# Performance work log

Hardware: AMD Instinct MI355X
Metric: run time of the kernel (lower is better)

The kernel has to match this reference:

```python
import jax, jax.numpy as jnp
import numpy as np

N, K, D = 32768, 8192, 256


def setup_inputs() -> dict:
    key = jax.random.key(0)
    k1, k2 = jax.random.split(key)
    x = jax.random.normal(k1, (N, D), dtype=jnp.float32)
    vectors = jax.random.normal(k2, (K, D), dtype=jnp.float32)  # codebook
    return {"x": x, "vectors": vectors}


def reference(x, vectors):
    # torch.cdist(x[:,None,:], vectors[None]) followed by argmin over K.
    # Euclidean distance is monotone in squared distance, so argmin over the
    # without a sqrt, matching the original math exactly for the returned ids.
    x2 = jnp.sum(x * x, axis=-1, keepdims=True)          # [N, 1]
    c2 = jnp.sum(vectors * vectors, axis=-1)             # [K]
    d2 = x2 + c2 - 2.0 * jnp.matmul(x, vectors.T)        # [N, K]
    indices = jnp.argmin(d2, axis=-1)                    # [N]
    return indices.astype(jnp.int32)
```

## Files before the change

kernel.cpp:

```cpp
#include <hip/hip_runtime.h>
#include <stdint.h>
#include <stddef.h>


#define N_PTS 32768
#define K_CB  8192
#define D_DIM 256
#define TM 128
#define TN 128
#define SPLITK 4
#define KCHUNK (K_CB / SPLITK)
#define NTILES (KCHUNK / TN)
#define NCHUNKS (NTILES * 8)

#define WS_XH   0
#define WS_XL   (WS_XH + N_PTS * D_DIM * 2)
#define WS_CH   (WS_XL + N_PTS * D_DIM * 2)
#define WS_CL   (WS_CH + K_CB * D_DIM * 2)
#define WS_C2   (WS_CL + K_CB * D_DIM * 2)
#define WS_PD   (WS_C2 + K_CB * 4)
#define WS_PI   (WS_PD + SPLITK * N_PTS * 4)
#define WS_END  (WS_PI + SPLITK * N_PTS * 4)

typedef _Float16 half4v __attribute__((ext_vector_type(4)));
typedef _Float16 half8v __attribute__((ext_vector_type(8)));
typedef float    f32x4  __attribute__((ext_vector_type(4)));

__device__ __forceinline__ void gld16(const void* g, void* l) {
    __builtin_amdgcn_global_load_lds(
        (const __attribute__((address_space(1))) void*)g,
        (__attribute__((address_space(3))) void*)l, 16, 0, 0);
}


#define XBLOCKS (N_PTS * D_DIM / 4 / 256)
#define CBLOCKS (K_CB * D_DIM / 4 / 256)

__global__ void __launch_bounds__(256)
prep_kernel(const float* __restrict__ x, const float* __restrict__ vecs,
            _Float16* __restrict__ xh, _Float16* __restrict__ xl,
            _Float16* __restrict__ ch, _Float16* __restrict__ cl,
            float* __restrict__ c2) {
    const int b = blockIdx.x;
    if (b < XBLOCKS) {
        const int i = b * 256 + threadIdx.x;
        const float4 v = ((const float4*)x)[i];
        half4v h = {(_Float16)v.x, (_Float16)v.y, (_Float16)v.z, (_Float16)v.w};
        half4v l = {(_Float16)((v.x - (float)h[0]) * 2048.0f),
                    (_Float16)((v.y - (float)h[1]) * 2048.0f),
                    (_Float16)((v.z - (float)h[2]) * 2048.0f),
                    (_Float16)((v.w - (float)h[3]) * 2048.0f)};
        *(half4v*)(xh + (size_t)i * 4) = h;
        *(half4v*)(xl + (size_t)i * 4) = l;
    } else {
        const int i = (b - XBLOCKS) * 256 + threadIdx.x;
        const float4 v = ((const float4*)vecs)[i];
        half4v h = {(_Float16)v.x, (_Float16)v.y, (_Float16)v.z, (_Float16)v.w};
        half4v l = {(_Float16)((v.x - (float)h[0]) * 2048.0f),
                    (_Float16)((v.y - (float)h[1]) * 2048.0f),
                    (_Float16)((v.z - (float)h[2]) * 2048.0f),
                    (_Float16)((v.w - (float)h[3]) * 2048.0f)};
        *(half4v*)(ch + (size_t)i * 4) = h;
        *(half4v*)(cl + (size_t)i * 4) = l;
        float s = v.x * v.x + v.y * v.y + v.z * v.z + v.w * v.w;
#pragma unroll
        for (int off = 32; off > 0; off >>= 1) s += __shfl_down(s, off, 64);
        if ((threadIdx.x & 63) == 0) c2[i >> 6] = s;
    }
}

__global__ void __launch_bounds__(256)
cnorms_kernel(const float* __restrict__ vecs, float* __restrict__ c2) {
    int gwave = (blockIdx.x * 256 + threadIdx.x) >> 6;
    int lane  = threadIdx.x & 63;
    const float* src = vecs + (size_t)gwave * D_DIM;
    float4 v = ((const float4*)src)[lane];
    float s = v.x * v.x + v.y * v.y + v.z * v.z + v.w * v.w;
#pragma unroll
    for (int off = 32; off > 0; off >>= 1) s += __shfl_down(s, off, 64);
    if (lane == 0) c2[gwave] = s;
}


__global__ void __launch_bounds__(256, 2)
vq_main_fast(const _Float16* __restrict__ xh_g, const _Float16* __restrict__ xl_g,
             const _Float16* __restrict__ ch_g, const _Float16* __restrict__ cl_g,
             const float* __restrict__ c2, float* __restrict__ pd, int* __restrict__ pi) {
    __shared__ __align__(16) char lds[32768];

    const int t    = threadIdx.x;
    const int lane = t & 63;
    const int wv   = t >> 6;
    const int wy   = wv >> 1, wx = wv & 1;
    const int fr   = lane & 15;
    const int g    = lane >> 4;

    const int split = blockIdx.x & (SPLITK - 1);
    const int pbase = (blockIdx.x >> 2) * TM;
    const int kbase = split * KCHUNK;

    const int srowoff = (lane >> 2) * (D_DIM * 2)
                      + ((((lane & 3) ^ ((lane >> 3) & 3))) << 4);
    const char* xh_s = (const char*)xh_g + (size_t)(pbase + wv * 32) * (D_DIM * 2) + srowoff;
    const char* xl_s = (const char*)xl_g + (size_t)(pbase + wv * 32) * (D_DIM * 2) + srowoff;
    const char* ch_s = (const char*)ch_g + (size_t)(kbase + wv * 32) * (D_DIM * 2) + srowoff;
    const char* cl_s = (const char*)cl_g + (size_t)(kbase + wv * 32) * (D_DIM * 2) + srowoff;
    const int stA = wv * 2048;

    const int skey = (fr >> 1) & 3;
    int aoff[4], boff[4];
#pragma unroll
    for (int i = 0; i < 4; ++i) {
        aoff[i] = (wy * 64 + i * 16 + fr) * 64 + ((g ^ skey) << 4);
        boff[i] = 16384 + (wx * 64 + i * 16 + fr) * 64 + ((g ^ skey) << 4);
    }

    f32x4 acc[4][4];

    auto STAGE = [&](int c) {
        const size_t kofs = (size_t)(c >> 3) * (TN * D_DIM * 2);
        const int gofs = (c & 7) * 64;
#pragma unroll
        for (int q = 0; q < 2; ++q) {
            gld16(xh_s + q * 8192 + gofs, lds +         stA + q * 1024);
            gld16(xl_s + q * 8192 + gofs, lds +  8192 + stA + q * 1024);
            gld16(ch_s + kofs + q * 8192 + gofs, lds + 16384 + stA + q * 1024);
            gld16(cl_s + kofs + q * 8192 + gofs, lds + 24576 + stA + q * 1024);
        }
    };

    auto COMPUTE = [&]() {
        half8v a1[4], a2[4], a3[4];
#pragma unroll
        for (int i = 0; i < 4; ++i) {
            const char* p = lds + aoff[i];
            a1[i] = *(const half8v*)p;
            a3[i] = *(const half8v*)(p + 8192);
            a2[i] = a1[i] * (_Float16)4.8828125e-4f;
        }
#pragma unroll
        for (int j = 0; j < 4; ++j) {
            const char* p = lds + boff[j];
            half8v b1 = *(const half8v*)p;
            half8v b2 = *(const half8v*)(p + 8192);
            half8v b3 = b1 * (_Float16)4.8828125e-4f;
#pragma unroll
            for (int i = 0; i < 4; ++i) {
                acc[i][j] = __builtin_amdgcn_mfma_f32_16x16x32_f16(a1[i], b1, acc[i][j], 0, 0, 0);
                acc[i][j] = __builtin_amdgcn_mfma_f32_16x16x32_f16(a2[i], b2, acc[i][j], 0, 0, 0);
                acc[i][j] = __builtin_amdgcn_mfma_f32_16x16x32_f16(a3[i], b3, acc[i][j], 0, 0, 0);
            }
        }
    };

    float best[16];
    int   bidx[16];
#pragma unroll
    for (int i = 0; i < 16; ++i) { best[i] = 3.4e38f; bidx[i] = 0; }

#pragma unroll 1
    for (int kt = 0; kt < NTILES; ++kt) {
#pragma unroll
        for (int i = 0; i < 4; ++i)
#pragma unroll
            for (int j = 0; j < 4; ++j) {
                f32x4 z = {0.f, 0.f, 0.f, 0.f};
                acc[i][j] = z;
            }

#pragma unroll 1
        for (int dkc = 0; dkc < 8; ++dkc) {
            const int c = kt * 8 + dkc;
            __syncthreads();
            STAGE(c);
            __syncthreads();
            COMPUTE();
        }

        const int ktbase = kbase + kt * TN;
#pragma unroll
        for (int j = 0; j < 4; ++j) {
            const int cg = ktbase + wx * 64 + j * 16 + fr;
            const float c2v = c2[cg];
#pragma unroll
            for (int i = 0; i < 4; ++i)
#pragma unroll
                for (int r = 0; r < 4; ++r) {
                    const float v = fmaf(-2.0f, acc[i][j][r], c2v);
                    const int s = i * 4 + r;
                    if (v < best[s]) { best[s] = v; bidx[s] = cg; }
                }
        }
    }

    __syncthreads();
    float* rd = (float*)lds;
    int*   ri = (int*)lds + 256;
#pragma unroll
    for (int i = 0; i < 4; ++i)
#pragma unroll
        for (int r = 0; r < 4; ++r) {
            float bv = best[i * 4 + r];
            int   bi = bidx[i * 4 + r];
#pragma unroll
            for (int off = 1; off < 16; off <<= 1) {
                const float ov = __shfl_xor(bv, off, 64);
                const int   oi = __shfl_xor(bi, off, 64);
                if (ov < bv || (ov == bv && oi < bi)) { bv = ov; bi = oi; }
            }
            if (fr == 0) {
                const int rowl = wy * 64 + i * 16 + g * 4 + r;
                rd[rowl * 2 + wx] = bv;
                ri[rowl * 2 + wx] = bi;
            }
        }
    __syncthreads();
    if (t < TM) {
        float b0 = rd[t * 2];
        int   i0 = ri[t * 2];
        const float b1 = rd[t * 2 + 1];
        const int   i1 = ri[t * 2 + 1];
        if (b1 < b0 || (b1 == b0 && i1 < i0)) { b0 = b1; i0 = i1; }
        pd[split * N_PTS + pbase + t] = b0;
        pi[split * N_PTS + pbase + t] = i0;
    }
}


#define BK 32
#define LS (BK + 4)

__device__ inline half8v load8(const _Float16* p) {
    half4v a = *(const half4v*)p;
    half4v b = *(const half4v*)(p + 4);
    return __builtin_shufflevector(a, b, 0, 1, 2, 3, 4, 5, 6, 7);
}

struct Trip { _Float16 h, s2, l2; };

__device__ inline Trip cvt3(float v) {
    Trip t;
    _Float16 hh = (_Float16)v;
    float hf = (float)hh;
    t.h  = hh;
    t.s2 = (_Float16)(hf * 4.8828125e-4f);
    t.l2 = (_Float16)((v - hf) * 2048.0f);
    return t;
}

__global__ void __launch_bounds__(256, 2)
vq_main_v3(const float* __restrict__ x, const float* __restrict__ vecs,
           const float* __restrict__ c2, float* __restrict__ pd, int* __restrict__ pi) {
    __shared__ _Float16 lds[6 * TM * LS];
    _Float16* xh  = lds;
    _Float16* xs2 = lds + 1 * TM * LS;
    _Float16* xl2 = lds + 2 * TM * LS;
    _Float16* ch  = lds + 3 * TM * LS;
    _Float16* cl2 = lds + 4 * TM * LS;
    _Float16* cs2 = lds + 5 * TM * LS;

    const int t     = threadIdx.x;
    const int split = blockIdx.x & (SPLITK - 1);
    const int pbase = (blockIdx.x >> 2) * TM;
    const int kbase = split * KCHUNK;

    const int lane = t & 63;
    const int wv   = t >> 6;
    const int wy   = wv >> 1, wx = wv & 1;
    const int fr   = lane & 15;
    const int g    = lane >> 4;
    const int kb   = g * 8;

    const int srow = t >> 3;
    const int sc4  = (t & 7) * 4;

    float best[16];
    int   bidx[16];
#pragma unroll
    for (int i = 0; i < 16; ++i) { best[i] = 3.4e38f; bidx[i] = 0; }

    for (int kt = 0; kt < NTILES; ++kt) {
        const int ktbase = kbase + kt * TN;
        f32x4 acc[4][4];
#pragma unroll
        for (int i = 0; i < 4; ++i)
#pragma unroll
            for (int j = 0; j < 4; ++j) {
                f32x4 z = {0.f, 0.f, 0.f, 0.f};
                acc[i][j] = z;
            }
        for (int dk = 0; dk < D_DIM; dk += BK) {
            __syncthreads();
#pragma unroll
            for (int p = 0; p < 4; ++p) {
                const int row = srow + p * 32;
                const float4 v = *(const float4*)&x[(size_t)(pbase + row) * D_DIM + dk + sc4];
                const Trip t0 = cvt3(v.x), t1 = cvt3(v.y), t2 = cvt3(v.z), t3 = cvt3(v.w);
                half4v h  = {t0.h,  t1.h,  t2.h,  t3.h};
                half4v s2 = {t0.s2, t1.s2, t2.s2, t3.s2};
                half4v l2 = {t0.l2, t1.l2, t2.l2, t3.l2};
                *(half4v*)&xh [row * LS + sc4] = h;
                *(half4v*)&xs2[row * LS + sc4] = s2;
                *(half4v*)&xl2[row * LS + sc4] = l2;
                const float4 w = *(const float4*)&vecs[(size_t)(ktbase + row) * D_DIM + dk + sc4];
                const Trip u0 = cvt3(w.x), u1 = cvt3(w.y), u2 = cvt3(w.z), u3 = cvt3(w.w);
                half4v hc = {u0.h,  u1.h,  u2.h,  u3.h};
                half4v sc = {u0.s2, u1.s2, u2.s2, u3.s2};
                half4v lc = {u0.l2, u1.l2, u2.l2, u3.l2};
                *(half4v*)&ch [row * LS + sc4] = hc;
                *(half4v*)&cs2[row * LS + sc4] = sc;
                *(half4v*)&cl2[row * LS + sc4] = lc;
            }
            __syncthreads();
            half8v a1[4], a2[4], a3[4], b1[4], b2[4], b3[4];
#pragma unroll
            for (int i = 0; i < 4; ++i) {
                const int aoff = (wy * 64 + i * 16 + fr) * LS + kb;
                a1[i] = load8(&xh [aoff]);
                a2[i] = load8(&xs2[aoff]);
                a3[i] = load8(&xl2[aoff]);
                const int boff2 = (wx * 64 + i * 16 + fr) * LS + kb;
                b1[i] = load8(&ch [boff2]);
                b2[i] = load8(&cl2[boff2]);
                b3[i] = load8(&cs2[boff2]);
            }
#pragma unroll
            for (int i = 0; i < 4; ++i)
#pragma unroll
                for (int j = 0; j < 4; ++j) {
                    acc[i][j] = __builtin_amdgcn_mfma_f32_16x16x32_f16(a1[i], b1[j], acc[i][j], 0, 0, 0);
                    acc[i][j] = __builtin_amdgcn_mfma_f32_16x16x32_f16(a2[i], b2[j], acc[i][j], 0, 0, 0);
                    acc[i][j] = __builtin_amdgcn_mfma_f32_16x16x32_f16(a3[i], b3[j], acc[i][j], 0, 0, 0);
                }
        }
#pragma unroll
        for (int j = 0; j < 4; ++j) {
            const int cg = ktbase + wx * 64 + j * 16 + fr;
            const float c2v = c2[cg];
#pragma unroll
            for (int i = 0; i < 4; ++i)
#pragma unroll
                for (int r = 0; r < 4; ++r) {
                    const float v = fmaf(-2.0f, acc[i][j][r], c2v);
                    const int s = i * 4 + r;
                    if (v < best[s]) { best[s] = v; bidx[s] = cg; }
                }
        }
    }
    __syncthreads();
    float* rd = (float*)lds;
    int*   ri = (int*)lds + 256;
#pragma unroll
    for (int i = 0; i < 4; ++i)
#pragma unroll
        for (int r = 0; r < 4; ++r) {
            float bv = best[i * 4 + r];
            int   bi = bidx[i * 4 + r];
#pragma unroll
            for (int off = 1; off < 16; off <<= 1) {
                const float ov = __shfl_xor(bv, off, 64);
                const int   oi = __shfl_xor(bi, off, 64);
                if (ov < bv || (ov == bv && oi < bi)) { bv = ov; bi = oi; }
            }
            if (fr == 0) {
                const int rowl = wy * 64 + i * 16 + g * 4 + r;
                rd[rowl * 2 + wx] = bv;
                ri[rowl * 2 + wx] = bi;
            }
        }
    __syncthreads();
    if (t < TM) {
        float b0 = rd[t * 2];
        int   i0 = ri[t * 2];
        const float b1 = rd[t * 2 + 1];
        const int   i1 = ri[t * 2 + 1];
        if (b1 < b0 || (b1 == b0 && i1 < i0)) { b0 = b1; i0 = i1; }
        pd[split * N_PTS + pbase + t] = b0;
        pi[split * N_PTS + pbase + t] = i0;
    }
}


__global__ void __launch_bounds__(256)
vq_combine(const float* __restrict__ pd, const int* __restrict__ pi,
           int* __restrict__ out) {
    const int p = blockIdx.x * 256 + threadIdx.x;
    float bb = pd[p];
    int   bi = pi[p];
#pragma unroll
    for (int s = 1; s < SPLITK; ++s) {
        const float v  = pd[s * N_PTS + p];
        const int   vi = pi[s * N_PTS + p];
        if (v < bb || (v == bb && vi < bi)) { bb = v; bi = vi; }
    }
    out[p] = bi;
}

extern "C" void kernel_launch(void* const* d_in, const int* in_sizes, int n_in,
                              void* d_out, int out_size, void* d_ws, size_t ws_size,
                              hipStream_t stream) {
    const float* x    = (const float*)d_in[0];
    const float* vecs = (const float*)d_in[1];
    int* out = (int*)d_out;
    char* ws = (char*)d_ws;

    if (ws_size >= (size_t)WS_END) {
        _Float16* xh = (_Float16*)(ws + WS_XH);
        _Float16* xl = (_Float16*)(ws + WS_XL);
        _Float16* ch = (_Float16*)(ws + WS_CH);
        _Float16* cl = (_Float16*)(ws + WS_CL);
        float* c2 = (float*)(ws + WS_C2);
        float* pd = (float*)(ws + WS_PD);
        int*   pi = (int*)(ws + WS_PI);

        hipLaunchKernelGGL(prep_kernel, dim3(XBLOCKS + CBLOCKS), dim3(256), 0, stream,
                           x, vecs, xh, xl, ch, cl, c2);
        hipLaunchKernelGGL(vq_main_fast, dim3((N_PTS / TM) * SPLITK), dim3(256), 0, stream,
                           xh, xl, ch, cl, c2, pd, pi);
        hipLaunchKernelGGL(vq_combine, dim3(N_PTS / 256), dim3(256), 0, stream,
                           pd, pi, out);
    } else {
        float* c2 = (float*)ws;
        float* pd = (float*)ws + K_CB;
        int*   pi = (int*)((float*)ws + K_CB + SPLITK * N_PTS);
        hipLaunchKernelGGL(cnorms_kernel, dim3(K_CB / 4), dim3(256), 0, stream,
                           vecs, c2);
        hipLaunchKernelGGL(vq_main_v3, dim3((N_PTS / TM) * SPLITK), dim3(256), 0, stream,
                           x, vecs, c2, pd, pi);
        hipLaunchKernelGGL(vq_combine, dim3(N_PTS / 256), dim3(256), 0, stream,
                           pd, pi, out);
    }
}
```

Baseline: 518.9 us.

## Load MFMA operands directly from global memory instead of staging through LDS

The main kernel drops the LDS staging (global_load_lds plus two barriers per chunk). Each wave now loads its fp16 hi/lo operand fragments straight from global memory into registers. This removes barrier and LDS traffic but gives up cross-wave data sharing: each operand is fetched by two waves, which raises global/L2 traffic. It also exposes load latency with no software pipelining.

After: 993.0 us. +91.4%, slower.

```diff
diff --git a/kernel.cpp b/kernel.cpp
--- a/kernel.cpp
+++ b/kernel.cpp
@@ -11,7 +11,6 @@
 #define SPLITK 4
 #define KCHUNK (K_CB / SPLITK)
 #define NTILES (KCHUNK / TN)
-#define NCHUNKS (NTILES * 8)
 
 #define WS_XH   0
 #define WS_XL   (WS_XH + N_PTS * D_DIM * 2)
@@ -25,12 +24,6 @@
 typedef _Float16 half4v __attribute__((ext_vector_type(4)));
 typedef _Float16 half8v __attribute__((ext_vector_type(8)));
 typedef float    f32x4  __attribute__((ext_vector_type(4)));
-
-__device__ __forceinline__ void gld16(const void* g, void* l) {
-    __builtin_amdgcn_global_load_lds(
-        (const __attribute__((address_space(1))) void*)g,
-        (__attribute__((address_space(3))) void*)l, 16, 0, 0);
-}
 
 
 #define XBLOCKS (N_PTS * D_DIM / 4 / 256)
@@ -86,7 +79,8 @@
 vq_main_fast(const _Float16* __restrict__ xh_g, const _Float16* __restrict__ xl_g,
              const _Float16* __restrict__ ch_g, const _Float16* __restrict__ cl_g,
              const float* __restrict__ c2, float* __restrict__ pd, int* __restrict__ pi) {
-    __shared__ __align__(16) char lds[32768];
+    __shared__ float rd[256];
+    __shared__ int   ri[256];
 
     const int t    = threadIdx.x;
     const int lane = t & 63;
@@ -99,59 +93,10 @@
     const int pbase = (blockIdx.x >> 2) * TM;
     const int kbase = split * KCHUNK;
 
-    const int srowoff = (lane >> 2) * (D_DIM * 2)
-                      + ((((lane & 3) ^ ((lane >> 3) & 3))) << 4);
-    const char* xh_s = (const char*)xh_g + (size_t)(pbase + wv * 32) * (D_DIM * 2) + srowoff;
-    const char* xl_s = (const char*)xl_g + (size_t)(pbase + wv * 32) * (D_DIM * 2) + srowoff;
-    const char* ch_s = (const char*)ch_g + (size_t)(kbase + wv * 32) * (D_DIM * 2) + srowoff;
-    const char* cl_s = (const char*)cl_g + (size_t)(kbase + wv * 32) * (D_DIM * 2) + srowoff;
-    const int stA = wv * 2048;
-
-    const int skey = (fr >> 1) & 3;
-    int aoff[4], boff[4];
-#pragma unroll
-    for (int i = 0; i < 4; ++i) {
-        aoff[i] = (wy * 64 + i * 16 + fr) * 64 + ((g ^ skey) << 4);
-        boff[i] = 16384 + (wx * 64 + i * 16 + fr) * 64 + ((g ^ skey) << 4);
-    }
-
-    f32x4 acc[4][4];
-
-    auto STAGE = [&](int c) {
-        const size_t kofs = (size_t)(c >> 3) * (TN * D_DIM * 2);
-        const int gofs = (c & 7) * 64;
-#pragma unroll
-        for (int q = 0; q < 2; ++q) {
-            gld16(xh_s + q * 8192 + gofs, lds +         stA + q * 1024);
-            gld16(xl_s + q * 8192 + gofs, lds +  8192 + stA + q * 1024);
-            gld16(ch_s + kofs + q * 8192 + gofs, lds + 16384 + stA + q * 1024);
-            gld16(cl_s + kofs + q * 8192 + gofs, lds + 24576 + stA + q * 1024);
-        }
-    };
-
-    auto COMPUTE = [&]() {
-        half8v a1[4], a2[4], a3[4];
-#pragma unroll
-        for (int i = 0; i < 4; ++i) {
-            const char* p = lds + aoff[i];
-            a1[i] = *(const half8v*)p;
-            a3[i] = *(const half8v*)(p + 8192);
-            a2[i] = a1[i] * (_Float16)4.8828125e-4f;
-        }
-#pragma unroll
-        for (int j = 0; j < 4; ++j) {
-            const char* p = lds + boff[j];
-            half8v b1 = *(const half8v*)p;
-            half8v b2 = *(const half8v*)(p + 8192);
-            half8v b3 = b1 * (_Float16)4.8828125e-4f;
-#pragma unroll
-            for (int i = 0; i < 4; ++i) {
-                acc[i][j] = __builtin_amdgcn_mfma_f32_16x16x32_f16(a1[i], b1, acc[i][j], 0, 0, 0);
-                acc[i][j] = __builtin_amdgcn_mfma_f32_16x16x32_f16(a2[i], b2, acc[i][j], 0, 0, 0);
-                acc[i][j] = __builtin_amdgcn_mfma_f32_16x16x32_f16(a3[i], b3, acc[i][j], 0, 0, 0);
-            }
-        }
-    };
+    const char* xhp = (const char*)xh_g + (size_t)(pbase + wy * 64 + fr) * 512 + g * 16;
+    const char* xlp = (const char*)xl_g + (size_t)(pbase + wy * 64 + fr) * 512 + g * 16;
+    const char* chp = (const char*)ch_g + (size_t)(kbase + wx * 64 + fr) * 512 + g * 16;
+    const char* clp = (const char*)cl_g + (size_t)(kbase + wx * 64 + fr) * 512 + g * 16;
 
     float best[16];
     int   bidx[16];
@@ -160,6 +105,9 @@
 
 #pragma unroll 1
     for (int kt = 0; kt < NTILES; ++kt) {
+        const size_t ktoff = (size_t)kt * (TN * 512);
+
+        f32x4 acc[4][4];
 #pragma unroll
         for (int i = 0; i < 4; ++i)
 #pragma unroll
@@ -170,11 +118,32 @@
 
 #pragma unroll 1
         for (int dkc = 0; dkc < 8; ++dkc) {
-            const int c = kt * 8 + dkc;
-            __syncthreads();
-            STAGE(c);
-            __syncthreads();
-            COMPUTE();
+            const int gofs = dkc * 64;
+            half8v a1[4], a3[4], b1[4], b2[4];
+#pragma unroll
+            for (int i = 0; i < 4; ++i) {
+                a1[i] = *(const half8v*)(xhp + i * 8192 + gofs);
+                a3[i] = *(const half8v*)(xlp + i * 8192 + gofs);
+            }
+#pragma unroll
+            for (int j = 0; j < 4; ++j) {
+                b1[j] = *(const half8v*)(chp + ktoff + j * 8192 + gofs);
+                b2[j] = *(const half8v*)(clp + ktoff + j * 8192 + gofs);
+            }
+            half8v a2[4];
+#pragma unroll
+            for (int i = 0; i < 4; ++i)
+                a2[i] = a1[i] * (_Float16)4.8828125e-4f;
+#pragma unroll
+            for (int j = 0; j < 4; ++j) {
+                half8v b3 = b1[j] * (_Float16)4.8828125e-4f;
+#pragma unroll
+                for (int i = 0; i < 4; ++i) {
+                    acc[i][j] = __builtin_amdgcn_mfma_f32_16x16x32_f16(a1[i], b1[j], acc[i][j], 0, 0, 0);
+                    acc[i][j] = __builtin_amdgcn_mfma_f32_16x16x32_f16(a2[i], b2[j], acc[i][j], 0, 0, 0);
+                    acc[i][j] = __builtin_amdgcn_mfma_f32_16x16x32_f16(a3[i], b3, acc[i][j], 0, 0, 0);
+                }
+            }
         }
 
         const int ktbase = kbase + kt * TN;
@@ -194,8 +163,6 @@
     }
 
     __syncthreads();
-    float* rd = (float*)lds;
-    int*   ri = (int*)lds + 256;
 #pragma unroll
     for (int i = 0; i < 4; ++i)
 #pragma unroll
```
